# Optimization experiments

Measured on AMD Instinct MI355X. Metric: run time of the kernel, lower is better.

## Reference

```python
import jax, jax.numpy as jnp
import numpy as np

B_, L_, H_, N_ = 8, 1024, 1024, 64

def setup_inputs() -> dict:
    key = jax.random.key(0)
    k1, k2, k3, k4 = jax.random.split(key, 4)
    return {
        "samples": jax.random.normal(k1, (B_, L_, 3 * H_), dtype=jnp.float32),
        "label_one_hot": jax.random.uniform(k2, (B_, L_, N_), dtype=jnp.float32),
        "predict": jax.random.normal(k3, (B_, L_, N_), dtype=jnp.float32),
        "W": jax.random.normal(k4, (H_, 3 * H_), dtype=jnp.float32) * (1.0 / np.sqrt(3 * H_)),
        "b_proj": jnp.zeros((H_,), dtype=jnp.float32),
    }

def reference(samples, label_one_hot, predict, W, b_proj):
    # projection: Linear(3H -> H)
    s = jnp.einsum("blk,hk->blh", samples, W) + b_proj          # [b,L,H]
    # dense similarity graph with diagonal masked out, row-softmax
    graph = jnp.einsum("blh,bmh->blm", s, s)                     # [b,L,L]
    L = graph.shape[1]
    eye = jnp.eye(L, dtype=graph.dtype)
    A = jax.nn.softmax(graph - 1e5 * eye, axis=-1)               # [b,L,L]
    # centered masked labels
    sup = label_one_hot
    row_has = (jnp.sum(sup, axis=-1) > 0.5).astype(sup.dtype)    # [b,L]
    total = jnp.sum(row_has, axis=-1)[:, None]                   # [b,1]
    avg = (jnp.sum(sup, axis=-2) / total)[:, None, :]            # [b,1,N]
    B0 = (sup - avg) * row_has[..., None]                        # [b,L,N]
    # diagonal inverse-degree scaling (elementwise, no dense diag matmul)
    d = 1.0 / (jnp.sum(A, axis=-1) + 1e-10)                      # [b,L]
    P = d[:, :, None] * jnp.swapaxes(A, -1, -2)                  # [b,L,L]
    Db = d[:, :, None] * B0                                      # [b,L,N]
    # 6-step power-iteration scan with residual injection at t==3
    ut = jnp.zeros_like(B0)
    for t in range(1, 7):
        ut = jnp.einsum("blm,bmn->bln", P, ut) + Db
        if t == 3:
            ut = ut + predict  # dropout is identity in eval mode
    return ut

if __name__ == "__main__":
    out = reference(**setup_inputs())
    print(out.shape, out.dtype)
```

## Files before the change

kernel.cpp:

```cpp
#include <hip/hip_runtime.h>


typedef _Float16 f16_t;
typedef f16_t f16x4 __attribute__((ext_vector_type(4)));
typedef f16_t f16x8 __attribute__((ext_vector_type(8)));
typedef float floatx4 __attribute__((ext_vector_type(4)));

__device__ __forceinline__ void async_copy16(const void* g, void* l) {
  __builtin_amdgcn_global_load_lds(
      (const __attribute__((address_space(1))) void*)g,
      (__attribute__((address_space(3))) void*)l, 16, 0, 0);
}

__device__ __forceinline__ f16_t hi_of(float x) { return (f16_t)x; }
__device__ __forceinline__ f16_t lo_of(float x, f16_t h) {
  return (f16_t)(x - (float)h);
}

__global__ __launch_bounds__(256) void prep_kernel(
    const float* __restrict__ W, f16_t* __restrict__ Whi, f16_t* __restrict__ Wlo,
    const float* __restrict__ samples, f16_t* __restrict__ SampH)
{
  const int bx = blockIdx.x, tid = threadIdx.x;
  if (bx < 3072) {
    const int i = bx * 256 + tid;
    float4 v = ((const float4*)W)[i];
    v.x *= 32.f; v.y *= 32.f; v.z *= 32.f; v.w *= 32.f;
    f16x4 h, l;
    f16_t h0 = hi_of(v.x); h[0] = h0; l[0] = lo_of(v.x, h0);
    f16_t h1 = hi_of(v.y); h[1] = h1; l[1] = lo_of(v.y, h1);
    f16_t h2 = hi_of(v.z); h[2] = h2; l[2] = lo_of(v.z, h2);
    f16_t h3 = hi_of(v.w); h[3] = h3; l[3] = lo_of(v.w, h3);
    *(f16x4*)(Whi + (size_t)i * 4) = h;
    *(f16x4*)(Wlo + (size_t)i * 4) = l;
  } else {
    const int i = (bx - 3072) * 256 + tid;
    const float4 v = ((const float4*)samples)[i];
    f16x4 h;
    h[0] = (f16_t)v.x; h[1] = (f16_t)v.y; h[2] = (f16_t)v.z; h[3] = (f16_t)v.w;
    *(f16x4*)(SampH + (size_t)i * 4) = h;
  }
}

struct Frags {
  f16x8 a[8];
  f16x8 bh0, bh1, bl0, bl1;
};

#define DSR(dst_, addr_, OFFSTR_) \
  asm volatile("ds_read_b128 %0, %1 offset:" OFFSTR_ : "=v"(dst_) : "v"(addr_))

__device__ __forceinline__ void read_frags_asm(unsigned sa, unsigned sb,
                                               Frags& f) {
  DSR(f.bh0, sb, "0");
  DSR(f.bh1, sb, "1024");
  DSR(f.bl0, sb, "8192");
  DSR(f.bl1, sb, "9216");
  DSR(f.a[0], sa, "0");
  DSR(f.a[1], sa, "1024");
  DSR(f.a[2], sa, "2048");
  DSR(f.a[3], sa, "3072");
  DSR(f.a[4], sa, "4096");
  DSR(f.a[5], sa, "5120");
  DSR(f.a[6], sa, "6144");
  DSR(f.a[7], sa, "7168");
}

__global__ __launch_bounds__(512, 2) void gemm1_pipe(
    const f16_t* __restrict__ Ag,
    const f16_t* __restrict__ BhG, const f16_t* __restrict__ BlG,
    const float* __restrict__ bias,
    f16_t* __restrict__ Chi, f16_t* __restrict__ Clo,
    int N, int K, float cscale)
{
  __shared__ __align__(16) char smem[131072];

  const int tid = threadIdx.x;
  const int lane = tid & 63;
  const int wave = tid >> 6;
  const int wm = wave >> 2;
  const int wn = wave & 3;
  const int m0 = blockIdx.y * 256;
  const int n0 = blockIdx.x * 128;
  const int fr = lane & 15;
  const int lch = lane >> 4;

  const int gA0 = tid;
  const int gA1 = tid + 512;
  const int rA0 = gA0 >> 2, lcA0 = (gA0 & 3) ^ ((rA0 >> 1) & 3);
  const int rA1 = gA1 >> 2, lcA1 = (gA1 & 3) ^ ((rA1 >> 1) & 3);
  const int rB = tid >> 2, lcB = (tid & 3) ^ ((rB >> 1) & 3);
  const f16_t* aSrc0 = Ag + (size_t)(m0 + rA0) * K + lcA0 * 8;
  const f16_t* aSrc1 = Ag + (size_t)(m0 + rA1) * K + lcA1 * 8;
  const f16_t* bhSrc = BhG + (size_t)(n0 + rB) * K + lcB * 8;
  const f16_t* blSrc = BlG + (size_t)(n0 + rB) * K + lcB * 8;
  char* ldsA0 = smem + gA0 * 16;
  char* ldsA1 = smem + gA1 * 16;
  char* ldsBh = smem + 16384 + (size_t)tid * 16;
  char* ldsBl = smem + 24576 + (size_t)tid * 16;

  const int swz = (lch ^ ((fr >> 1) & 3)) * 16;
  const int aoff = (wm * 128 + fr) * 64 + swz;
  const int boff = (wn * 32 + fr) * 64 + swz;
  const unsigned ldsBase =
      (unsigned)(size_t)(__attribute__((address_space(3))) char*)smem;
  const unsigned aA0 = ldsBase + (unsigned)aoff;
  const unsigned aA1 = aA0 + 32768u;
  const unsigned aA2 = aA0 + 65536u;
  const unsigned aA3 = aA0 + 98304u;
  const unsigned bA0 = ldsBase + 16384u + (unsigned)boff;
  const unsigned bA1 = bA0 + 32768u;
  const unsigned bA2 = bA0 + 65536u;
  const unsigned bA3 = bA0 + 98304u;

  floatx4 acc[8][2] = {};
  const int NS = K >> 5;

#define STAGE(SS_, SLOT_)                                     \
  do {                                                        \
    int ss = (SS_); if (ss >= NS) ss -= NS;                   \
    const int k0 = ss * 32;                                   \
    async_copy16(aSrc0 + k0, ldsA0 + (SLOT_) * 32768);        \
    async_copy16(aSrc1 + k0, ldsA1 + (SLOT_) * 32768);        \
    async_copy16(bhSrc + k0, ldsBh + (SLOT_) * 32768);        \
    async_copy16(blSrc + k0, ldsBl + (SLOT_) * 32768);        \
  } while (0)

#define MFMA8(F_, P_)                                                                                               \
  do {                                                                                                              \
    acc[2*(P_)][0]   = __builtin_amdgcn_mfma_f32_16x16x32_f16((F_).a[2*(P_)],   (F_).bh0, acc[2*(P_)][0],   0,0,0); \
    acc[2*(P_)][1]   = __builtin_amdgcn_mfma_f32_16x16x32_f16((F_).a[2*(P_)],   (F_).bh1, acc[2*(P_)][1],   0,0,0); \
    acc[2*(P_)+1][0] = __builtin_amdgcn_mfma_f32_16x16x32_f16((F_).a[2*(P_)+1], (F_).bh0, acc[2*(P_)+1][0], 0,0,0); \
    acc[2*(P_)+1][1] = __builtin_amdgcn_mfma_f32_16x16x32_f16((F_).a[2*(P_)+1], (F_).bh1, acc[2*(P_)+1][1], 0,0,0); \
    acc[2*(P_)][0]   = __builtin_amdgcn_mfma_f32_16x16x32_f16((F_).a[2*(P_)],   (F_).bl0, acc[2*(P_)][0],   0,0,0); \
    acc[2*(P_)][1]   = __builtin_amdgcn_mfma_f32_16x16x32_f16((F_).a[2*(P_)],   (F_).bl1, acc[2*(P_)][1],   0,0,0); \
    acc[2*(P_)+1][0] = __builtin_amdgcn_mfma_f32_16x16x32_f16((F_).a[2*(P_)+1], (F_).bl0, acc[2*(P_)+1][0], 0,0,0); \
    acc[2*(P_)+1][1] = __builtin_amdgcn_mfma_f32_16x16x32_f16((F_).a[2*(P_)+1], (F_).bl1, acc[2*(P_)+1][1], 0,0,0); \
  } while (0)

#define SB0 __builtin_amdgcn_sched_barrier(0)

#define HALF(SPRE_, SLOTPRE_, ARD_, BRD_, FRD_, FMM_)            \
  do {                                                           \
    STAGE(SPRE_, SLOTPRE_);                                      \
    asm volatile("s_waitcnt vmcnt(8)" ::: "memory");             \
    __builtin_amdgcn_s_barrier();                                \
    DSR(FRD_.bh0, BRD_, "0");                                    \
    DSR(FRD_.bh1, BRD_, "1024");                                 \
    DSR(FRD_.bl0, BRD_, "8192");                                 \
    SB0;                                                         \
    asm volatile("s_waitcnt lgkmcnt(3)" ::: "memory");           \
    SB0;                                                         \
    __builtin_amdgcn_s_setprio(1);                               \
    MFMA8(FMM_, 0);                                              \
    __builtin_amdgcn_s_setprio(0);                               \
    SB0;                                                         \
    DSR(FRD_.bl1, BRD_, "9216");                                 \
    DSR(FRD_.a[0], ARD_, "0");                                   \
    DSR(FRD_.a[1], ARD_, "1024");                                \
    SB0;                                                         \
    __builtin_amdgcn_s_setprio(1);                               \
    MFMA8(FMM_, 1);                                              \
    __builtin_amdgcn_s_setprio(0);                               \
    SB0;                                                         \
    DSR(FRD_.a[2], ARD_, "2048");                                \
    DSR(FRD_.a[3], ARD_, "3072");                                \
    DSR(FRD_.a[4], ARD_, "4096");                                \
    SB0;                                                         \
    __builtin_amdgcn_s_setprio(1);                               \
    MFMA8(FMM_, 2);                                              \
    __builtin_amdgcn_s_setprio(0);                               \
    SB0;                                                         \
    DSR(FRD_.a[5], ARD_, "5120");                                \
    DSR(FRD_.a[6], ARD_, "6144");                                \
    DSR(FRD_.a[7], ARD_, "7168");                                \
    SB0;                                                         \
    __builtin_amdgcn_s_setprio(1);                               \
    MFMA8(FMM_, 3);                                              \
    __builtin_amdgcn_s_setprio(0);                               \
    SB0;                                                         \
  } while (0)

  Frags f0, f1;

  STAGE(0, 0); STAGE(1, 1); STAGE(2, 2);
  asm volatile("s_waitcnt vmcnt(8)" ::: "memory");
  __builtin_amdgcn_s_barrier();
  read_frags_asm(aA0, bA0, f0);
  SB0;

  for (int s = 0; s < NS; s += 4) {
    HALF(s + 3, 3, aA1, bA1, f1, f0);
    HALF(s + 4, 0, aA2, bA2, f0, f1);
    HALF(s + 5, 1, aA3, bA3, f1, f0);
    HALF(s + 6, 2, aA0, bA0, f0, f1);
  }
  asm volatile("s_waitcnt vmcnt(0)" ::: "memory");
#undef HALF
#undef STAGE
#undef MFMA8

  const int mr = (lane >> 4) * 4;
#pragma unroll
  for (int j = 0; j < 2; ++j) {
    const int n = n0 + wn * 32 + j * 16 + fr;
    const float bj = bias[n];
#pragma unroll
    for (int i = 0; i < 8; ++i) {
#pragma unroll
      for (int r = 0; r < 4; ++r) {
        const int m = m0 + wm * 128 + i * 16 + mr + r;
        float v = acc[i][j][r] * cscale + bj;
        f16_t h = hi_of(v);
        Chi[(size_t)m * N + n] = h;
        Clo[(size_t)m * N + n] = lo_of(v, h);
      }
    }
  }
}

template <int CMODE>
__global__ __launch_bounds__(256) void gemm_mfma(
    const f16_t* __restrict__ AhiG,
    const f16_t* __restrict__ BhiG, const f16_t* __restrict__ BloG,
    const float* __restrict__ bias,
    float* __restrict__ Cf, f16_t* __restrict__ Chi, f16_t* __restrict__ Clo,
    int M, int N, int K, long long sA, long long sB, long long sC, float cscale)
{
  AhiG += (long long)blockIdx.z * sA;
  BhiG += (long long)blockIdx.z * sB;
  BloG += (long long)blockIdx.z * sB;
  if (CMODE == 1) Cf += (long long)blockIdx.z * sC;

  __shared__ __align__(16) char smem[49152];
  f16_t* AsHi = (f16_t*)smem;
  f16_t* BsHi = (f16_t*)(smem + 16384);
  f16_t* BsLo = (f16_t*)(smem + 32768);

  const int tid = threadIdx.x;
  const int lane = tid & 63;
  const int wave = tid >> 6;
  const int wm = wave >> 1, wn = wave & 1;

  int m0, n0;
  if (CMODE == 0) {
    m0 = blockIdx.y * 128;
    n0 = blockIdx.x * 128;
  } else {
    int idx = blockIdx.x, i = 0, accu = 0;
    while (accu + i + 1 <= idx) { accu += i + 1; ++i; }
    m0 = i * 128;
    n0 = (idx - accu) * 128;
  }

  const int fr = lane & 15;
  const int kg = ((lane >> 4) ^ ((fr >> 1) & 3)) * 8;
  const int aoff = (wm * 64 + fr) * 32 + kg;
  const int boff = (wn * 64 + fr) * 32 + kg;

  floatx4 acc[4][4] = {};

  for (int k0 = 0; k0 < K; k0 += 64) {
    __syncthreads();
#pragma unroll
    for (int it = 0; it < 4; ++it) {
      const int cb = it * 256 + wave * 64;
      const int c = cb + lane;
      const int kk = c >> 9;
      const int row = (c >> 2) & 127;
      const int kc = kk * 32 + (((c & 3) ^ ((row >> 1) & 3)) * 8);
      const size_t ga = (size_t)(m0 + row) * K + k0 + kc;
      const size_t gb = (size_t)(n0 + row) * K + k0 + kc;
      async_copy16(AhiG + ga, (char*)AsHi + (size_t)cb * 16);
      async_copy16(BhiG + gb, (char*)BsHi + (size_t)cb * 16);
      async_copy16(BloG + gb, (char*)BsLo + (size_t)cb * 16);
    }
    __syncthreads();

#pragma unroll
    for (int kk = 0; kk < 2; ++kk) {
      f16x8 ah[4], bh[4], bl[4];
#pragma unroll
      for (int t = 0; t < 4; ++t) {
        ah[t] = *(const f16x8*)&AsHi[kk * 4096 + aoff + t * 512];
        bh[t] = *(const f16x8*)&BsHi[kk * 4096 + boff + t * 512];
        bl[t] = *(const f16x8*)&BsLo[kk * 4096 + boff + t * 512];
      }
#pragma unroll
      for (int i = 0; i < 4; ++i)
#pragma unroll
        for (int j = 0; j < 4; ++j) {
          acc[i][j] = __builtin_amdgcn_mfma_f32_16x16x32_f16(ah[i], bh[j], acc[i][j], 0, 0, 0);
          acc[i][j] = __builtin_amdgcn_mfma_f32_16x16x32_f16(ah[i], bl[j], acc[i][j], 0, 0, 0);
        }
    }
  }

  const int mr = (lane >> 4) * 4;
#pragma unroll
  for (int j = 0; j < 4; ++j) {
    const int n = n0 + wn * 64 + j * 16 + fr;
    const float bj = (CMODE == 0) ? bias[n] : 0.f;
#pragma unroll
    for (int i = 0; i < 4; ++i) {
#pragma unroll
      for (int r = 0; r < 4; ++r) {
        const int m = m0 + wm * 64 + i * 16 + mr + r;
        float v = acc[i][j][r];
        if (CMODE == 0) {
          v = v * cscale + bj;
          f16_t h = hi_of(v);
          Chi[(size_t)m * N + n] = h;
          Clo[(size_t)m * N + n] = lo_of(v, h);
        } else {
          if (m == n) v -= 1e5f;
          Cf[(size_t)m * N + n] = v;
        }
      }
    }
  }

  if (CMODE == 1 && m0 != n0) {
    float* T = (float*)smem;
#pragma unroll
    for (int mc = 0; mc < 4; ++mc) {
      __syncthreads();
      if (wm == (mc >> 1)) {
        const int ibase = (mc & 1) * 2;
#pragma unroll
        for (int di = 0; di < 2; ++di) {
#pragma unroll
          for (int j = 0; j < 4; ++j) {
            const int nl = wn * 64 + j * 16 + fr;
#pragma unroll
            for (int r = 0; r < 4; ++r) {
              const int mloc = di * 16 + mr + r;
              T[nl * 36 + mloc] = acc[ibase + di][j][r];
            }
          }
        }
      }
      __syncthreads();
      const int row = tid >> 1, half = tid & 1;
      const float* src = &T[row * 36 + half * 16];
      float* dst = Cf + (size_t)(n0 + row) * N + m0 + mc * 32 + half * 16;
#pragma unroll
      for (int q = 0; q < 16; ++q) dst[q] = src[q];
    }
  }
}

__global__ __launch_bounds__(256) void rowstats_kernel(
    const float* __restrict__ G, float* __restrict__ mx, float* __restrict__ inv)
{
  __shared__ float red[4];
  const int tid = threadIdx.x;
  const float* g = G + (size_t)blockIdx.x * 1024;
  const float4 v = ((const float4*)g)[tid];

  float m = fmaxf(fmaxf(v.x, v.y), fmaxf(v.z, v.w));
#pragma unroll
  for (int off = 32; off > 0; off >>= 1) m = fmaxf(m, __shfl_down(m, off));
  if ((tid & 63) == 0) red[tid >> 6] = m;
  __syncthreads();
  m = fmaxf(fmaxf(red[0], red[1]), fmaxf(red[2], red[3]));
  __syncthreads();

  float s = __expf(v.x - m) + __expf(v.y - m) + __expf(v.z - m) + __expf(v.w - m);
#pragma unroll
  for (int off = 32; off > 0; off >>= 1) s += __shfl_down(s, off);
  if ((tid & 63) == 0) red[tid >> 6] = s;
  __syncthreads();
  if (tid == 0) {
    mx[blockIdx.x] = m;
    inv[blockIdx.x] = 1.0f / (red[0] + red[1] + red[2] + red[3]);
  }
}

__global__ __launch_bounds__(256) void make_at_kernel(
    const float* __restrict__ G, const float* __restrict__ mx,
    const float* __restrict__ inv, f16_t* __restrict__ At)
{
  const int row = blockIdx.x;
  const int b = row >> 10;
  const int tid = threadIdx.x;
  const float4 g = ((const float4*)(G + (size_t)row * 1024))[tid];
  const float4 m = ((const float4*)(mx + b * 1024))[tid];
  const float4 iv = ((const float4*)(inv + b * 1024))[tid];
  f16x4 o;
  o[0] = (f16_t)(__expf(g.x - m.x) * iv.x);
  o[1] = (f16_t)(__expf(g.y - m.y) * iv.y);
  o[2] = (f16_t)(__expf(g.z - m.z) * iv.z);
  o[3] = (f16_t)(__expf(g.w - m.w) * iv.w);
  *(f16x4*)(At + (size_t)row * 1024 + tid * 4) = o;
}

__global__ __launch_bounds__(1024) void make_db_kernel(
    const float* __restrict__ sup, float* __restrict__ Db, f16_t* __restrict__ DbT)
{
  const int L = 1024, Nn = 64;
  const float* s = sup + (size_t)blockIdx.x * L * Nn;
  float* db = Db + (size_t)blockIdx.x * L * Nn;
  f16_t* dbt = DbT + (size_t)blockIdx.x * L * Nn;
  __shared__ float rowhas[1024];
  __shared__ float cpart[1024];
  __shared__ float tpart[16];
  __shared__ float avg[64];
  __shared__ float totalsh;
  const int tid = threadIdx.x;

  const float4* sr = (const float4*)(s + (size_t)tid * 64);
  float ss = 0.f;
#pragma unroll
  for (int i = 0; i < 16; ++i) { const float4 v = sr[i]; ss += (v.x + v.y) + (v.z + v.w); }
  const float rh = (ss > 0.5f) ? 1.f : 0.f;
  rowhas[tid] = rh;
  float t = rh;
#pragma unroll
  for (int off = 32; off > 0; off >>= 1) t += __shfl_down(t, off);
  if ((tid & 63) == 0) tpart[tid >> 6] = t;

  const int n = tid & 63, seg = tid >> 6;
  float cs = 0.f;
  for (int l = seg * 64; l < seg * 64 + 64; ++l) cs += s[(size_t)l * 64 + n];
  cpart[seg * 64 + n] = cs;
  __syncthreads();
  if (tid == 0) { float tt = 0.f; for (int i = 0; i < 16; ++i) tt += tpart[i]; totalsh = tt; }
  __syncthreads();
  if (tid < 64) {
    float a = 0.f;
    for (int i = 0; i < 16; ++i) a += cpart[i * 64 + tid];
    avg[tid] = a / totalsh;
  }
  __syncthreads();

  const float4* s4 = (const float4*)s;
  float4* d4 = (float4*)db;
  for (int i = tid; i < (L * Nn) / 4; i += 1024) {
    float4 v = s4[i];
    const int l = i >> 4;
    const int nb = (i & 15) * 4;
    const float rhl = rowhas[l];
    v.x = (v.x - avg[nb + 0]) * rhl;
    v.y = (v.y - avg[nb + 1]) * rhl;
    v.z = (v.z - avg[nb + 2]) * rhl;
    v.w = (v.w - avg[nb + 3]) * rhl;
    d4[i] = v;
  }
  for (int i = tid; i < L * Nn; i += 1024) {
    const int n2 = i >> 10, l2 = i & 1023;
    dbt[i] = (f16_t)((s[(size_t)l2 * 64 + n2] - avg[n2]) * rowhas[l2]);
  }
}

template <int PRED, int FINAL>
__global__ __launch_bounds__(256) void iter_step(
    const f16_t* __restrict__ At, const f16_t* __restrict__ UT,
    const float* __restrict__ Db, const float* __restrict__ Pred,
    f16_t* __restrict__ UTn, float* __restrict__ OutF)
{
  const int L = 1024, Nn = 64;
  const int b = blockIdx.y, l0 = blockIdx.x * 32;
  At += (size_t)b * L * L;
  UT += (size_t)b * Nn * L;

  __shared__ __align__(16) char smem[131072];

  const int tid = threadIdx.x;
  const int lane = tid & 63;
  const int wave = tid >> 6;
  const int fr = lane & 15;
  const int lch = lane >> 4;
  const int mwb = wave * 256;

  int g_, rw_, sc_;
  g_ = lane;        rw_ = g_ >> 3; sc_ = (g_ & 7) ^ (rw_ & 7);
  const f16_t* aS0 = At + (size_t)(l0 + rw_) * L + mwb + sc_ * 8;
  g_ = lane + 64;   rw_ = g_ >> 3; sc_ = (g_ & 7) ^ (rw_ & 7);
  const f16_t* aS1 = At + (size_t)(l0 + rw_) * L + mwb + sc_ * 8;
  g_ = lane + 128;  rw_ = g_ >> 3; sc_ = (g_ & 7) ^ (rw_ & 7);
  const f16_t* aS2 = At + (size_t)(l0 + rw_) * L + mwb + sc_ * 8;
  g_ = lane + 192;  rw_ = g_ >> 3; sc_ = (g_ & 7) ^ (rw_ & 7);
  const f16_t* aS3 = At + (size_t)(l0 + rw_) * L + mwb + sc_ * 8;
  g_ = lane;        rw_ = g_ >> 3; sc_ = (g_ & 7) ^ (rw_ & 7);
  const f16_t* uS0 = UT + (size_t)rw_ * L + mwb + sc_ * 8;
  g_ = lane + 64;   rw_ = g_ >> 3; sc_ = (g_ & 7) ^ (rw_ & 7);
  const f16_t* uS1 = UT + (size_t)rw_ * L + mwb + sc_ * 8;
  g_ = lane + 128;  rw_ = g_ >> 3; sc_ = (g_ & 7) ^ (rw_ & 7);
  const f16_t* uS2 = UT + (size_t)rw_ * L + mwb + sc_ * 8;
  g_ = lane + 192;  rw_ = g_ >> 3; sc_ = (g_ & 7) ^ (rw_ & 7);
  const f16_t* uS3 = UT + (size_t)rw_ * L + mwb + sc_ * 8;
  g_ = lane + 256;  rw_ = g_ >> 3; sc_ = (g_ & 7) ^ (rw_ & 7);
  const f16_t* uS4 = UT + (size_t)rw_ * L + mwb + sc_ * 8;
  g_ = lane + 320;  rw_ = g_ >> 3; sc_ = (g_ & 7) ^ (rw_ & 7);
  const f16_t* uS5 = UT + (size_t)rw_ * L + mwb + sc_ * 8;
  g_ = lane + 384;  rw_ = g_ >> 3; sc_ = (g_ & 7) ^ (rw_ & 7);
  const f16_t* uS6 = UT + (size_t)rw_ * L + mwb + sc_ * 8;
  g_ = lane + 448;  rw_ = g_ >> 3; sc_ = (g_ & 7) ^ (rw_ & 7);
  const f16_t* uS7 = UT + (size_t)rw_ * L + mwb + sc_ * 8;

  char* stA = smem + wave * 24576;
  char* stU = stA + 4096;

  const int offK0 = fr * 128 + ((lch ^ (fr & 7)) * 16);
  const int offK1 = fr * 128 + (((4 + lch) ^ (fr & 7)) * 16);

  floatx4 acc[2][4] = {};

#define STG(M0_, BUF_)                                        \
  do {                                                        \
    char* dA = stA + (BUF_) * 12288;                          \
    char* dU = stU + (BUF_) * 12288;                          \
    async_copy16(aS0 + (M0_), dA + lane * 16);                \
    async_copy16(aS1 + (M0_), dA + 1024 + lane * 16);         \
    async_copy16(aS2 + (M0_), dA + 2048 + lane * 16);         \
    async_copy16(aS3 + (M0_), dA + 3072 + lane * 16);         \
    async_copy16(uS0 + (M0_), dU + lane * 16);                \
    async_copy16(uS1 + (M0_), dU + 1024 + lane * 16);         \
    async_copy16(uS2 + (M0_), dU + 2048 + lane * 16);         \
    async_copy16(uS3 + (M0_), dU + 3072 + lane * 16);         \
    async_copy16(uS4 + (M0_), dU + 4096 + lane * 16);         \
    async_copy16(uS5 + (M0_), dU + 5120 + lane * 16);         \
    async_copy16(uS6 + (M0_), dU + 6144 + lane * 16);         \
    async_copy16(uS7 + (M0_), dU + 7168 + lane * 16);         \
  } while (0)

#define LD8(b_, o_) (*(const f16x8*)((b_) + (o_)))
#define MM(A_, U_, C_) C_ = __builtin_amdgcn_mfma_f32_16x16x32_f16(A_, U_, C_, 0, 0, 0)

#define CHUNK(BUF_)                                                       \
  do {                                                                    \
    const char* cA = stA + (BUF_) * 12288;                                \
    const char* cU = stU + (BUF_) * 12288;                                \
    f16x8 a00 = LD8(cA, offK0), a01 = LD8(cA, offK1);                     \
    f16x8 a10 = LD8(cA, offK0 + 2048), a11 = LD8(cA, offK1 + 2048);       \
    f16x8 u00 = LD8(cU, offK0), u01 = LD8(cU, offK1);                     \
    f16x8 u10 = LD8(cU, offK0 + 2048), u11 = LD8(cU, offK1 + 2048);       \
    f16x8 u20 = LD8(cU, offK0 + 4096), u21 = LD8(cU, offK1 + 4096);       \
    f16x8 u30 = LD8(cU, offK0 + 6144), u31 = LD8(cU, offK1 + 6144);       \
    MM(a00, u00, acc[0][0]); MM(a00, u10, acc[0][1]);                     \
    MM(a00, u20, acc[0][2]); MM(a00, u30, acc[0][3]);                     \
    MM(a10, u00, acc[1][0]); MM(a10, u10, acc[1][1]);                     \
    MM(a10, u20, acc[1][2]); MM(a10, u30, acc[1][3]);                     \
    MM(a01, u01, acc[0][0]); MM(a01, u11, acc[0][1]);                     \
    MM(a01, u21, acc[0][2]); MM(a01, u31, acc[0][3]);                     \
    MM(a11, u01, acc[1][0]); MM(a11, u11, acc[1][1]);                     \
    MM(a11, u21, acc[1][2]); MM(a11, u31, acc[1][3]);                     \
  } while (0)

#define SB0 __builtin_amdgcn_sched_barrier(0)

  STG(0, 0);
  STG(64, 1);
  asm volatile("s_waitcnt vmcnt(12)" ::: "memory");
  SB0;
  CHUNK(0);
  SB0;
  STG(128, 0);
  asm volatile("s_waitcnt vmcnt(12)" ::: "memory");
  SB0;
  CHUNK(1);
  SB0;
  STG(192, 1);
  asm volatile("s_waitcnt vmcnt(12)" ::: "memory");
  SB0;
  CHUNK(0);
  SB0;
  asm volatile("s_waitcnt vmcnt(0)" ::: "memory");
  SB0;
  CHUNK(1);
#undef CHUNK
#undef STG

  float* P = (float*)(smem + 98304) + wave * 2048;
  const int mr = (lane >> 4) * 4;
#pragma unroll
  for (int li = 0; li < 2; ++li)
#pragma unroll
    for (int j = 0; j < 4; ++j)
#pragma unroll
      for (int r = 0; r < 4; ++r)
        P[(li * 16 + mr + r) * 64 + j * 16 + fr] = acc[li][j][r];
  __syncthreads();

  const float* P0 = (const float*)(smem + 98304);
  const size_t obase = ((size_t)b * L + l0) * Nn;
  f16_t* OutS = (f16_t*)smem;
#pragma unroll
  for (int it = 0; it < 2; ++it) {
    const int e4 = it * 256 + tid;
    const int l = e4 >> 4, n4 = (e4 & 15) * 4;
    const int eo = l * 64 + n4;
    float4 v = *(const float4*)(P0 + eo);
    const float4 p1 = *(const float4*)(P0 + 2048 + eo);
    const float4 p2 = *(const float4*)(P0 + 4096 + eo);
    const float4 p3 = *(const float4*)(P0 + 6144 + eo);
    v.x += p1.x; v.y += p1.y; v.z += p1.z; v.w += p1.w;
    v.x += p2.x; v.y += p2.y; v.z += p2.z; v.w += p2.w;
    v.x += p3.x; v.y += p3.y; v.z += p3.z; v.w += p3.w;
    const float4 d = *(const float4*)(Db + obase + eo);
    v.x += d.x; v.y += d.y; v.z += d.z; v.w += d.w;
    if (PRED) {
      const float4 p = *(const float4*)(Pred + obase + eo);
      v.x += p.x; v.y += p.y; v.z += p.z; v.w += p.w;
    }
    if (FINAL) {
      *(float4*)(OutF + obase + eo) = v;
    } else {
      OutS[(n4 + 0) * 40 + l] = (f16_t)v.x;
      OutS[(n4 + 1) * 40 + l] = (f16_t)v.y;
      OutS[(n4 + 2) * 40 + l] = (f16_t)v.z;
      OutS[(n4 + 3) * 40 + l] = (f16_t)v.w;
    }
  }
  if (!FINAL) {
    __syncthreads();
    f16_t* dst = UTn + (size_t)b * Nn * L + l0;
    const int n = tid >> 2, lc = (tid & 3) * 8;
    *(f16x8*)(dst + (size_t)n * L + lc) = *(const f16x8*)&OutS[n * 40 + lc];
  }
#undef SB0
#undef LD8
#undef MM
}

extern "C" void kernel_launch(void* const* d_in, const int* in_sizes, int n_in,
                              void* d_out, int out_size, void* d_ws, size_t ws_size,
                              hipStream_t stream) {
  const float* samples = (const float*)d_in[0];
  const float* label   = (const float*)d_in[1];
  const float* predict = (const float*)d_in[2];
  const float* W       = (const float*)d_in[3];
  const float* bproj   = (const float*)d_in[4];
  float* out = (float*)d_out;

  char* ws = (char*)d_ws;
  f16_t* Whi = (f16_t*)ws;
  f16_t* Wlo = (f16_t*)(ws + 6291456);
  float* mx  = (float*)ws;
  float* inv = (float*)(ws + 32768);
  float* Db  = (float*)(ws + 65536);
  f16_t* DbT = (f16_t*)(ws + 65536 + 2097152);
  f16_t* UTa = (f16_t*)(ws + 65536 + 3145728);
  f16_t* UTb = (f16_t*)(ws + 65536 + 4194304);
  f16_t* SampH = (f16_t*)(ws + 12582912);
  float* G     = (float*)(ws + 12582912);
  f16_t* Shi = (f16_t*)(ws + 62914560);
  f16_t* Slo = (f16_t*)(ws + 62914560 + 16777216);
  f16_t* At  = Shi;

  const long long LH = 1024LL * 1024;
  const long long LL = 1024LL * 1024;

  prep_kernel<<<dim3(27648), 256, 0, stream>>>(W, Whi, Wlo, samples, SampH);

  gemm1_pipe<<<dim3(8, 32), 512, 0, stream>>>(
      SampH, Whi, Wlo, bproj, Shi, Slo, 1024, 3072, 1.0f / 32.0f);

  gemm_mfma<1><<<dim3(36, 1, 8), 256, 0, stream>>>(
      Shi, Shi, Slo, nullptr, G, nullptr, nullptr,
      1024, 1024, 1024, LH, LH, LL, 1.0f);

  rowstats_kernel<<<8192, 256, 0, stream>>>(G, mx, inv);
  make_at_kernel<<<8192, 256, 0, stream>>>(G, mx, inv, At);

  make_db_kernel<<<8, 1024, 0, stream>>>(label, Db, DbT);

  dim3 gi(32, 8);
  iter_step<0, 0><<<gi, 256, 0, stream>>>(At, DbT, Db, nullptr, UTa, nullptr);
  iter_step<1, 0><<<gi, 256, 0, stream>>>(At, UTa, Db, predict, UTb, nullptr);
  iter_step<0, 0><<<gi, 256, 0, stream>>>(At, UTb, Db, nullptr, UTa, nullptr);
  iter_step<0, 0><<<gi, 256, 0, stream>>>(At, UTa, Db, nullptr, UTb, nullptr);
  iter_step<0, 1><<<gi, 256, 0, stream>>>(At, UTb, Db, nullptr, nullptr, out);
}
```

Baseline: 388.3 us.

## Software-pipeline the Gram GEMM with 4-slot LDS ring and swizzle GEMM1 block order

Replaces the generic synchronous gemm_mfma used for the S·Sᵀ Gram matrix with a dedicated kernel that keeps a 4-slot LDS ring of async global→LDS copies and interleaves LDS fragment reads with MFMA groups under sched barriers and priority hints. This is meant to hide global load latency and LDS read latency that the old two-barrier-per-K-step loop exposed. GEMM1's block index is also remapped so that concurrently running blocks share A/B tiles for better L2 reuse. The new kernel uses 96 KB of LDS with one block per CU and hand-tuned waitcnt counts, which is fragile.

```diff
diff --git a/kernel.cpp b/kernel.cpp
--- a/kernel.cpp
+++ b/kernel.cpp
@@ -80,8 +80,10 @@
   const int wave = tid >> 6;
   const int wm = wave >> 2;
   const int wn = wave & 3;
-  const int m0 = blockIdx.y * 256;
-  const int n0 = blockIdx.x * 128;
+  const int bid0 = blockIdx.y * 8 + blockIdx.x;
+  const int xk = bid0 & 7, xj = bid0 >> 3;
+  const int m0 = ((xk >> 1) * 8 + (xj >> 2)) * 256;
+  const int n0 = ((xk & 1) * 4 + (xj & 3)) * 128;
   const int fr = lane & 15;
   const int lch = lane >> 4;
 
@@ -219,108 +221,185 @@
   }
 }
 
-template <int CMODE>
-__global__ __launch_bounds__(256) void gemm_mfma(
-    const f16_t* __restrict__ AhiG,
-    const f16_t* __restrict__ BhiG, const f16_t* __restrict__ BloG,
-    const float* __restrict__ bias,
-    float* __restrict__ Cf, f16_t* __restrict__ Chi, f16_t* __restrict__ Clo,
-    int M, int N, int K, long long sA, long long sB, long long sC, float cscale)
+struct Frags2 {
+  f16x8 a[4];
+  f16x8 bh[4];
+  f16x8 bl[4];
+};
+
+__global__ __launch_bounds__(256, 1) void gemm2_pipe(
+    const f16_t* __restrict__ Sh, const f16_t* __restrict__ Sl,
+    float* __restrict__ Gf)
 {
-  AhiG += (long long)blockIdx.z * sA;
-  BhiG += (long long)blockIdx.z * sB;
-  BloG += (long long)blockIdx.z * sB;
-  if (CMODE == 1) Cf += (long long)blockIdx.z * sC;
-
-  __shared__ __align__(16) char smem[49152];
-  f16_t* AsHi = (f16_t*)smem;
-  f16_t* BsHi = (f16_t*)(smem + 16384);
-  f16_t* BsLo = (f16_t*)(smem + 32768);
+  const int K = 1024, N = 1024;
+  const long long bo = (long long)blockIdx.z * (1024LL * 1024);
+  const f16_t* Ahi = Sh + bo;
+  const f16_t* Bhi = Sh + bo;
+  const f16_t* Blo = Sl + bo;
+  float* Cf = Gf + bo;
+
+  __shared__ __align__(16) char smem[98304];
 
   const int tid = threadIdx.x;
   const int lane = tid & 63;
   const int wave = tid >> 6;
   const int wm = wave >> 1, wn = wave & 1;
 
-  int m0, n0;
-  if (CMODE == 0) {
-    m0 = blockIdx.y * 128;
-    n0 = blockIdx.x * 128;
-  } else {
-    int idx = blockIdx.x, i = 0, accu = 0;
-    while (accu + i + 1 <= idx) { accu += i + 1; ++i; }
-    m0 = i * 128;
-    n0 = (idx - accu) * 128;
-  }
+  int idx = blockIdx.x, ti = 0, accu = 0;
+  while (accu + ti + 1 <= idx) { accu += ti + 1; ++ti; }
+  const int m0 = ti * 128;
+  const int n0 = (idx - accu) * 128;
 
   const int fr = lane & 15;
-  const int kg = ((lane >> 4) ^ ((fr >> 1) & 3)) * 8;
-  const int aoff = (wm * 64 + fr) * 32 + kg;
-  const int boff = (wn * 64 + fr) * 32 + kg;
+  const int lch = lane >> 4;
+
+  const int gA0 = tid, gA1 = tid + 256;
+  const int rA0 = gA0 >> 2, cA0 = (gA0 & 3) ^ ((rA0 >> 1) & 3);
+  const int rA1 = gA1 >> 2, cA1 = (gA1 & 3) ^ ((rA1 >> 1) & 3);
+  const f16_t* aSr0 = Ahi + (size_t)(m0 + rA0) * K + cA0 * 8;
+  const f16_t* aSr1 = Ahi + (size_t)(m0 + rA1) * K + cA1 * 8;
+  const f16_t* hSr0 = Bhi + (size_t)(n0 + rA0) * K + cA0 * 8;
+  const f16_t* hSr1 = Bhi + (size_t)(n0 + rA1) * K + cA1 * 8;
+  const f16_t* lSr0 = Blo + (size_t)(n0 + rA0) * K + cA0 * 8;
+  const f16_t* lSr1 = Blo + (size_t)(n0 + rA1) * K + cA1 * 8;
+  char* dA0 = smem + gA0 * 16;
+  char* dA1 = smem + gA1 * 16;
+  char* dH0 = smem + 8192 + gA0 * 16;
+  char* dH1 = smem + 8192 + gA1 * 16;
+  char* dL0 = smem + 16384 + gA0 * 16;
+  char* dL1 = smem + 16384 + gA1 * 16;
+
+  const int swz16 = (lch ^ ((fr >> 1) & 3)) * 16;
+  const int aoff = (wm * 64 + fr) * 64 + swz16;
+  const int boff = (wn * 64 + fr) * 64 + swz16;
+  const unsigned ldsBase =
+      (unsigned)(size_t)(__attribute__((address_space(3))) char*)smem;
+  const unsigned aS0 = ldsBase + (unsigned)aoff;
+  const unsigned aS1 = aS0 + 24576u;
+  const unsigned aS2 = aS0 + 49152u;
+  const unsigned aS3 = aS0 + 73728u;
+  const unsigned bS0 = ldsBase + 8192u + (unsigned)boff;
+  const unsigned bS1 = bS0 + 24576u;
+  const unsigned bS2 = bS0 + 49152u;
+  const unsigned bS3 = bS0 + 73728u;
 
   floatx4 acc[4][4] = {};
-
-  for (int k0 = 0; k0 < K; k0 += 64) {
-    __syncthreads();
-#pragma unroll
-    for (int it = 0; it < 4; ++it) {
-      const int cb = it * 256 + wave * 64;
-      const int c = cb + lane;
-      const int kk = c >> 9;
-      const int row = (c >> 2) & 127;
-      const int kc = kk * 32 + (((c & 3) ^ ((row >> 1) & 3)) * 8);
-      const size_t ga = (size_t)(m0 + row) * K + k0 + kc;
-      const size_t gb = (size_t)(n0 + row) * K + k0 + kc;
-      async_copy16(AhiG + ga, (char*)AsHi + (size_t)cb * 16);
-      async_copy16(BhiG + gb, (char*)BsHi + (size_t)cb * 16);
-      async_copy16(BloG + gb, (char*)BsLo + (size_t)cb * 16);
-    }
-    __syncthreads();
-
-#pragma unroll
-    for (int kk = 0; kk < 2; ++kk) {
-      f16x8 ah[4], bh[4], bl[4];
-#pragma unroll
-      for (int t = 0; t < 4; ++t) {
-        ah[t] = *(const f16x8*)&AsHi[kk * 4096 + aoff + t * 512];
-        bh[t] = *(const f16x8*)&BsHi[kk * 4096 + boff + t * 512];
-        bl[t] = *(const f16x8*)&BsLo[kk * 4096 + boff + t * 512];
-      }
-#pragma unroll
-      for (int i = 0; i < 4; ++i)
-#pragma unroll
-        for (int j = 0; j < 4; ++j) {
-          acc[i][j] = __builtin_amdgcn_mfma_f32_16x16x32_f16(ah[i], bh[j], acc[i][j], 0, 0, 0);
-          acc[i][j] = __builtin_amdgcn_mfma_f32_16x16x32_f16(ah[i], bl[j], acc[i][j], 0, 0, 0);
-        }
-    }
-  }
+  const int NS = 32;
+
+#define STAGE2(SS_, SLOT_)                                    \
+  do {                                                        \
+    int ss = (SS_); if (ss >= NS) ss -= NS;                   \
+    const int k0 = ss * 32;                                   \
+    async_copy16(aSr0 + k0, dA0 + (SLOT_) * 24576);           \
+    async_copy16(aSr1 + k0, dA1 + (SLOT_) * 24576);           \
+    async_copy16(hSr0 + k0, dH0 + (SLOT_) * 24576);           \
+    async_copy16(hSr1 + k0, dH1 + (SLOT_) * 24576);           \
+    async_copy16(lSr0 + k0, dL0 + (SLOT_) * 24576);           \
+    async_copy16(lSr1 + k0, dL1 + (SLOT_) * 24576);           \
+  } while (0)
+
+#define MFMA8_2(F_, P_)                                                                              \
+  do {                                                                                               \
+    acc[0][P_] = __builtin_amdgcn_mfma_f32_16x16x32_f16((F_).a[0], (F_).bh[P_], acc[0][P_], 0,0,0);  \
+    acc[1][P_] = __builtin_amdgcn_mfma_f32_16x16x32_f16((F_).a[1], (F_).bh[P_], acc[1][P_], 0,0,0);  \
+    acc[2][P_] = __builtin_amdgcn_mfma_f32_16x16x32_f16((F_).a[2], (F_).bh[P_], acc[2][P_], 0,0,0);  \
+    acc[3][P_] = __builtin_amdgcn_mfma_f32_16x16x32_f16((F_).a[3], (F_).bh[P_], acc[3][P_], 0,0,0);  \
+    acc[0][P_] = __builtin_amdgcn_mfma_f32_16x16x32_f16((F_).a[0], (F_).bl[P_], acc[0][P_], 0,0,0);  \
+    acc[1][P_] = __builtin_amdgcn_mfma_f32_16x16x32_f16((F_).a[1], (F_).bl[P_], acc[1][P_], 0,0,0);  \
+    acc[2][P_] = __builtin_amdgcn_mfma_f32_16x16x32_f16((F_).a[2], (F_).bl[P_], acc[2][P_], 0,0,0);  \
+    acc[3][P_] = __builtin_amdgcn_mfma_f32_16x16x32_f16((F_).a[3], (F_).bl[P_], acc[3][P_], 0,0,0);  \
+  } while (0)
+
+#define SB0 __builtin_amdgcn_sched_barrier(0)
+
+#define GR2(SPRE_, SLOTPRE_, ARD_, BRD_, FRD_, FMM_)             \
+  do {                                                           \
+    STAGE2(SPRE_, SLOTPRE_);                                     \
+    asm volatile("s_waitcnt vmcnt(12)" ::: "memory");            \
+    __builtin_amdgcn_s_barrier();                                \
+    DSR(FRD_.bh[0], BRD_, "0");                                  \
+    DSR(FRD_.bh[1], BRD_, "1024");                               \
+    DSR(FRD_.bh[2], BRD_, "2048");                               \
+    SB0;                                                         \
+    asm volatile("s_waitcnt lgkmcnt(3)" ::: "memory");           \
+    SB0;                                                         \
+    __builtin_amdgcn_s_setprio(1);                               \
+    MFMA8_2(FMM_, 0);                                            \
+    __builtin_amdgcn_s_setprio(0);                               \
+    SB0;                                                         \
+    DSR(FRD_.bh[3], BRD_, "3072");                               \
+    DSR(FRD_.bl[0], BRD_, "8192");                               \
+    DSR(FRD_.bl[1], BRD_, "9216");                               \
+    SB0;                                                         \
+    __builtin_amdgcn_s_setprio(1);                               \
+    MFMA8_2(FMM_, 1);                                            \
+    __builtin_amdgcn_s_setprio(0);                               \
+    SB0;                                                         \
+    DSR(FRD_.bl[2], BRD_, "10240");                              \
+    DSR(FRD_.bl[3], BRD_, "11264");                              \
+    DSR(FRD_.a[0], ARD_, "0");                                   \
+    SB0;                                                         \
+    __builtin_amdgcn_s_setprio(1);                               \
+    MFMA8_2(FMM_, 2);                                            \
+    __builtin_amdgcn_s_setprio(0);                               \
+    SB0;                                                         \
+    DSR(FRD_.a[1], ARD_, "1024");                                \
+    DSR(FRD_.a[2], ARD_, "2048");                                \
+    DSR(FRD_.a[3], ARD_, "3072");                                \
+    SB0;                                                         \
+    __builtin_amdgcn_s_setprio(1);                               \
+    MFMA8_2(FMM_, 3);                                            \
+    __builtin_amdgcn_s_setprio(0);                               \
+    SB0;                                                         \
+  } while (0)
+
+  Frags2 f0, f1;
+
+  STAGE2(0, 0); STAGE2(1, 1); STAGE2(2, 2);
+  asm volatile("s_waitcnt vmcnt(12)" ::: "memory");
+  __builtin_amdgcn_s_barrier();
+  DSR(f0.bh[0], bS0, "0");
+  DSR(f0.bh[1], bS0, "1024");
+  DSR(f0.bh[2], bS0, "2048");
+  DSR(f0.bh[3], bS0, "3072");
+  DSR(f0.bl[0], bS0, "8192");
+  DSR(f0.bl[1], bS0, "9216");
+  DSR(f0.bl[2], bS0, "10240");
+  DSR(f0.bl[3], bS0, "11264");
+  DSR(f0.a[0], aS0, "0");
+  DSR(f0.a[1], aS0, "1024");
+  DSR(f0.a[2], aS0, "2048");
+  DSR(f0.a[3], aS0, "3072");
+  SB0;
+
+  for (int s = 0; s < NS; s += 4) {
+    GR2(s + 3, 3, aS1, bS1, f1, f0);
+    GR2(s + 4, 0, aS2, bS2, f0, f1);
+    GR2(s + 5, 1, aS3, bS3, f1, f0);
+    GR2(s + 6, 2, aS0, bS0, f0, f1);
+  }
+  asm volatile("s_waitcnt vmcnt(0)" ::: "memory");
+#undef GR2
+#undef MFMA8_2
+#undef STAGE2
 
   const int mr = (lane >> 4) * 4;
 #pragma unroll
   for (int j = 0; j < 4; ++j) {
     const int n = n0 + wn * 64 + j * 16 + fr;
-    const float bj = (CMODE == 0) ? bias[n] : 0.f;
 #pragma unroll
     for (int i = 0; i < 4; ++i) {
 #pragma unroll
       for (int r = 0; r < 4; ++r) {
         const int m = m0 + wm * 64 + i * 16 + mr + r;
         float v = acc[i][j][r];
-        if (CMODE == 0) {
-          v = v * cscale + bj;
-          f16_t h = hi_of(v);
-          Chi[(size_t)m * N + n] = h;
-          Clo[(size_t)m * N + n] = lo_of(v, h);
-        } else {
-          if (m == n) v -= 1e5f;
-          Cf[(size_t)m * N + n] = v;
-        }
+        if (m == n) v -= 1e5f;
+        Cf[(size_t)m * N + n] = v;
       }
     }
   }
 
-  if (CMODE == 1 && m0 != n0) {
+  if (m0 != n0) {
     float* T = (float*)smem;
 #pragma unroll
     for (int mc = 0; mc < 4; ++mc) {
@@ -649,17 +728,12 @@
   f16_t* Slo = (f16_t*)(ws + 62914560 + 16777216);
   f16_t* At  = Shi;
 
-  const long long LH = 1024LL * 1024;
-  const long long LL = 1024LL * 1024;
-
   prep_kernel<<<dim3(27648), 256, 0, stream>>>(W, Whi, Wlo, samples, SampH);
 
   gemm1_pipe<<<dim3(8, 32), 512, 0, stream>>>(
       SampH, Whi, Wlo, bproj, Shi, Slo, 1024, 3072, 1.0f / 32.0f);
 
-  gemm_mfma<1><<<dim3(36, 1, 8), 256, 0, stream>>>(
-      Shi, Shi, Slo, nullptr, G, nullptr, nullptr,
-      1024, 1024, 1024, LH, LH, LL, 1.0f);
+  gemm2_pipe<<<dim3(36, 1, 8), 256, 0, stream>>>(Shi, Slo, G);
 
   rowstats_kernel<<<8192, 256, 0, stream>>>(G, mx, inv);
   make_at_kernel<<<8192, 256, 0, stream>>>(G, mx, inv, At);
```

After: 382.0 us. No clear change (-1.6%).
